# Optimization experiments

Hardware: AMD Instinct MI355X
Metric: run time of the kernel (lower is better)

## Reference

```python
import jax, jax.numpy as jnp
import numpy as np

N = 50000      # nodes
E = 800000     # edges (avg degree 16)
IN, HID, OUT = 128, 256, 64
G = 500        # graphs in the batch (100 nodes each)
NEG_SLOPE = 0.01
EPS = 1e-12


def setup_inputs() -> dict:
    key = jax.random.key(0)
    ks = jax.random.split(key, 9)
    x = jax.random.normal(ks[0], (N, IN), jnp.float32)
    edge_index = jax.random.randint(ks[1], (2, E), 0, N, dtype=jnp.int32)
    # sorted segment ids with every graph present (100 nodes per graph)
    batch = jnp.repeat(jnp.arange(G, dtype=jnp.int32), N // G)
    def lin(k, fan_in, fan_out):
        s = 1.0 / np.sqrt(fan_in)
        kw, kb = jax.random.split(k)
        W = jax.random.uniform(kw, (fan_in, fan_out), jnp.float32, -s, s)
        b = jax.random.uniform(kb, (fan_out,), jnp.float32, -s, s)
        return W, b
    W1, b1 = lin(ks[2], IN, HID)
    W2, b2 = lin(ks[3], HID, HID)
    W3, b3 = lin(ks[4], HID, OUT)
    return {"x": x, "edge_index": edge_index, "batch": batch,
            "W1": W1, "b1": b1, "W2": W2, "b2": b2, "W3": W3, "b3": b3}


def _sage_conv(x, edge_index, W, b):
    # SAGEConv(aggr='add', root_weight=False, normalize=True):
    # gather source features, scatter-add to targets, linear, L2 normalize.
    src, dst = edge_index[0], edge_index[1]
    agg = jax.ops.segment_sum(x[src], dst, num_segments=x.shape[0])  # [N, d_in]
    out = agg @ W + b                                                 # [N, d_out]
    nrm = jnp.linalg.norm(out, axis=-1, keepdims=True)
    return out / jnp.maximum(nrm, EPS)


def reference(x, edge_index, batch, W1, b1, W2, b2, W3, b3):
    h = _sage_conv(x, edge_index, W1, b1)
    h = jax.nn.leaky_relu(h, NEG_SLOPE)          # dropout p=0 -> identity
    h = _sage_conv(h, edge_index, W2, b2)
    h = jax.nn.leaky_relu(h, NEG_SLOPE)
    h = _sage_conv(h, edge_index, W3, b3)
    # get_zero_nodes: first node of each graph (batch sorted, all G present)
    mask = jnp.concatenate([jnp.ones((1,), bool), batch[1:] != batch[:-1]])
    first_idx = jnp.nonzero(mask, size=G)[0]
    return h[first_idx]                          # [G, OUT]
```

## Files before the change

kernel.cpp:

```cpp
#include <hip/hip_runtime.h>

#define N_NODES 50000
#define E_EDGES 800000
#define IN_DIM  128
#define HID_DIM 256
#define OUT_DIM 64
#define G_GRAPHS 500
#define CAP 64
#define NBINS 196
#define BINCAP 5120

typedef __attribute__((ext_vector_type(8))) short short8;
typedef __attribute__((ext_vector_type(4))) float float4v;

__device__ __forceinline__ float bf2f(unsigned short u) {
  union { unsigned int i; float f; } c; c.i = ((unsigned int)u) << 16; return c.f;
}
__device__ __forceinline__ unsigned short f2bf(float f) {
  union { float f; unsigned int i; } c; c.f = f;
  unsigned int x = c.i;
  x += 0x7FFFu + ((x >> 16) & 1u);
  return (unsigned short)(x >> 16);
}
__device__ __forceinline__ unsigned int fbits(float f) {
  union { float f; unsigned int i; } c; c.f = f; return c.i;
}
__device__ __forceinline__ float bits2f(unsigned int u) {
  union { unsigned int i; float f; } c; c.i = u; return c.f;
}


__global__ __launch_bounds__(256) void prep1(
    const int* __restrict__ src, const int* __restrict__ dst,
    const int* __restrict__ batch,
    const float* __restrict__ x,
    const float* __restrict__ W1, const float* __restrict__ W2,
    unsigned int* __restrict__ binbuf, int* __restrict__ bin_next,
    int* __restrict__ first_node,
    unsigned short* __restrict__ xb,
    unsigned short* __restrict__ W1t, unsigned short* __restrict__ W2t) {
  const int b = blockIdx.x, tid = threadIdx.x;
  if (b < 200) {
    __shared__ int cnt[NBINS];
    __shared__ int gbase[NBINS];
    for (int i = tid; i < NBINS; i += 256) cnt[i] = 0;
    __syncthreads();
    const int base = b * 4096;
    unsigned int pk[16]; int bp[16];
#pragma unroll
    for (int u = 0; u < 16; ++u) {
      const int e = base + u * 256 + tid;
      bp[u] = -1;
      if (e < E_EDGES) {
        const int d = dst[e];
        const int s = src[e];
        const int bin = d >> 8;
        const int pos = atomicAdd(&cnt[bin], 1);
        pk[u] = ((unsigned int)(d & 255) << 16) | (unsigned int)s;
        bp[u] = (bin << 16) | pos;
      }
    }
    __syncthreads();
    for (int i = tid; i < NBINS; i += 256)
      gbase[i] = atomicAdd(&bin_next[i], cnt[i]);
    __syncthreads();
#pragma unroll
    for (int u = 0; u < 16; ++u) {
      if (bp[u] >= 0) {
        const int bin = bp[u] >> 16, pos = bp[u] & 0xFFFF;
        const int idx = gbase[bin] + pos;
        if (idx < BINCAP) binbuf[bin * BINCAP + idx] = pk[u];
      }
    }
  } else if (b < 6450) {
    const int t = (b - 200) * 256 + tid;
    const int i = t * 4;
    const float4 v = *(const float4*)(x + i);
    ushort4 u;
    u.x = f2bf(v.x); u.y = f2bf(v.y); u.z = f2bf(v.z); u.w = f2bf(v.w);
    *(ushort4*)(xb + i) = u;
    if (t < N_NODES) {
      if (t == 0 || batch[t] != batch[t - 1]) first_node[batch[t]] = t;
    }
  } else {
    const int t = (b - 6450) * 256 + tid;
    if (t < 8192) {
      const int n = t >> 5, k0 = (t & 31) * 4;
      ushort4 o;
      o.x = f2bf(W1[(k0 + 0) * 256 + n]);
      o.y = f2bf(W1[(k0 + 1) * 256 + n]);
      o.z = f2bf(W1[(k0 + 2) * 256 + n]);
      o.w = f2bf(W1[(k0 + 3) * 256 + n]);
      *(ushort4*)&W1t[n * 128 + k0] = o;
    } else {
      const int v2 = t - 8192;
      const int n = v2 >> 6, k0 = (v2 & 63) * 4;
      ushort4 o;
      o.x = f2bf(W2[(k0 + 0) * 256 + n]);
      o.y = f2bf(W2[(k0 + 1) * 256 + n]);
      o.z = f2bf(W2[(k0 + 2) * 256 + n]);
      o.w = f2bf(W2[(k0 + 3) * 256 + n]);
      *(ushort4*)&W2t[n * 256 + k0] = o;
    }
  }
}


__global__ __launch_bounds__(512) void prep2(
    const unsigned int* __restrict__ binbuf, const int* __restrict__ bin_next,
    int* __restrict__ deg, unsigned short* __restrict__ srcs) {
  __shared__ unsigned short img[256 * CAP];
  __shared__ int cnt[256];
  const int tid = threadIdx.x;
  const int bin = blockIdx.x;
  if (tid < 256) cnt[tid] = 0;
  __syncthreads();
  const int total = min(bin_next[bin], BINCAP);
  const unsigned int* bb = binbuf + bin * BINCAP;
  for (int i = tid; i < total; i += 512) {
    const unsigned int pk = bb[i];
    const int nl = pk >> 16;
    const int pos = atomicAdd(&cnt[nl], 1);
    if (pos < CAP) img[(nl << 6) + pos] = (unsigned short)(pk & 0xFFFFu);
  }
  __syncthreads();
  const int node0 = bin << 8;
  const int nend = min(N_NODES, node0 + 256);
  if (tid < 256 && node0 + tid < nend) deg[node0 + tid] = cnt[tid];
  const int nwords = (nend - node0) * 32;
  unsigned int* dstw = (unsigned int*)(srcs + ((size_t)node0 << 6));
  const unsigned int* srcw = (const unsigned int*)img;
  for (int i = tid; i < nwords; i += 512) dstw[i] = srcw[i];
}


__global__ __launch_bounds__(64) void build_list2(
    const int* __restrict__ deg, const unsigned short* __restrict__ srcs,
    const int* __restrict__ first_node,
    unsigned char* __restrict__ need1, int* __restrict__ list2,
    int* __restrict__ cnt2) {
  const int g = blockIdx.x;
  const int lane = threadIdx.x;
  const int node = first_node[g];
  const int cnt = min(deg[node], CAP);
  int s = 0;
  if (lane < cnt) s = srcs[(node << 6) + lane];
  const unsigned long long m = __ballot(lane < cnt);
  int base = 0;
  if (lane == 0) base = atomicAdd(cnt2, __popcll(m));
  base = __shfl(base, 0);
  if (lane < cnt) {
    list2[base + lane] = s;
    const int c2 = min(deg[s], CAP);
    for (int q = 0; q < c2; ++q) need1[srcs[(s << 6) + q]] = 1;
  }
}

__global__ __launch_bounds__(256) void compact_list1(
    const unsigned char* __restrict__ need1,
    int* __restrict__ list1, int* __restrict__ cnt1) {
  __shared__ int wbase[4];
  const int tid = threadIdx.x;
  const int lane = tid & 63;
  const int wv = tid >> 6;
  const int i = blockIdx.x * 256 + tid;
  const bool f = (i < N_NODES) && need1[i];
  const unsigned long long m = __ballot(f);
  if (lane == 0) wbase[wv] = __popcll(m);
  __syncthreads();
  if (tid == 0) {
    const int t0 = wbase[0], t1 = wbase[1], t2 = wbase[2], t3 = wbase[3];
    const int b = atomicAdd(cnt1, t0 + t1 + t2 + t3);
    wbase[0] = b; wbase[1] = b + t0; wbase[2] = b + t0 + t1; wbase[3] = b + t0 + t1 + t2;
  }
  __syncthreads();
  if (f) list1[wbase[wv] + __popcll(m & ((1ull << lane) - 1ull))] = i;
}


template<int K>
__global__ __launch_bounds__(512, 8) void fused_layer(
    const unsigned short* __restrict__ H,
    const int* __restrict__ deg, const unsigned short* __restrict__ srcs,
    const unsigned short* __restrict__ Wt,
    const float* __restrict__ bias,
    unsigned short* __restrict__ Hout,
    const int* __restrict__ nodelist,
    const int* __restrict__ pcount)
{
  constexpr int M = 256;
  constexpr int TN = 16;
  constexpr int VPT = K / 64;
  constexpr int LDK = K + 8;
  __shared__ unsigned short a_hi[TN][LDK];
  __shared__ unsigned short a_lo[TN][LDK];
  __shared__ float ssq_tot[TN];
  __shared__ int nid_s[TN];
  const int tid = threadIdx.x;
  const int lane = tid & 63;
  const int wv = tid >> 6;

  const int total = __builtin_amdgcn_readfirstlane(*pcount);
  if (blockIdx.x * TN >= total) return;

  if (tid < TN) {
    int gi = blockIdx.x * TN + tid;
    if (gi >= total) gi = total - 1;
    nid_s[tid] = nodelist[gi];
    ssq_tot[tid] = 0.f;
  }
  __syncthreads();

  const unsigned short* hb = H + lane * VPT;
  const int node0 = __builtin_amdgcn_readfirstlane(nid_s[2 * wv]);
  const int node1 = __builtin_amdgcn_readfirstlane(nid_s[2 * wv + 1]);
  const int cnt0 = __builtin_amdgcn_readfirstlane(min(deg[node0], CAP));
  const int cnt1 = __builtin_amdgcn_readfirstlane(min(deg[node1], CAP));
  int idx0 = 0, idx1 = 0;
  if (lane < cnt0) idx0 = srcs[(node0 << 6) + lane];
  if (lane < cnt1) idx1 = srcs[(node1 << 6) + lane];

#pragma unroll
  for (int i = 0; i < 2; ++i) {
    const int nn = 2 * wv + i;
    const int cnt = i ? cnt1 : cnt0;
    const int idx = i ? idx1 : idx0;

    float acc[VPT];
#pragma unroll
    for (int j = 0; j < VPT; ++j) acc[j] = 0.f;

    int j = 0;
    for (; j + 16 <= cnt; j += 16) {
      int s[16];
#pragma unroll
      for (int u = 0; u < 16; ++u) s[u] = __builtin_amdgcn_readlane(idx, j + u);
      if constexpr (VPT == 4) {
        ushort4 r[16];
#pragma unroll
        for (int u = 0; u < 16; ++u) r[u] = *(const ushort4*)(hb + s[u] * K);
#pragma unroll
        for (int u = 0; u < 16; ++u) {
          acc[0] += bf2f(r[u].x); acc[1] += bf2f(r[u].y);
          acc[2] += bf2f(r[u].z); acc[3] += bf2f(r[u].w);
        }
      } else {
        ushort2 r[16];
#pragma unroll
        for (int u = 0; u < 16; ++u) r[u] = *(const ushort2*)(hb + s[u] * K);
#pragma unroll
        for (int u = 0; u < 16; ++u) {
          acc[0] += bf2f(r[u].x); acc[1] += bf2f(r[u].y);
        }
      }
    }
    for (; j < cnt; j += 8) {
      int s[8]; float w[8];
#pragma unroll
      for (int u = 0; u < 8; ++u) {
        const int q = j + u;
        const int qm = (q < cnt) ? q : (cnt - 1);
        s[u] = __builtin_amdgcn_readlane(idx, qm);
        w[u] = (q < cnt) ? 1.f : 0.f;
      }
      if constexpr (VPT == 4) {
        ushort4 r[8];
#pragma unroll
        for (int u = 0; u < 8; ++u) r[u] = *(const ushort4*)(hb + s[u] * K);
#pragma unroll
        for (int u = 0; u < 8; ++u) {
          acc[0] = fmaf(w[u], bf2f(r[u].x), acc[0]);
          acc[1] = fmaf(w[u], bf2f(r[u].y), acc[1]);
          acc[2] = fmaf(w[u], bf2f(r[u].z), acc[2]);
          acc[3] = fmaf(w[u], bf2f(r[u].w), acc[3]);
        }
      } else {
        ushort2 r[8];
#pragma unroll
        for (int u = 0; u < 8; ++u) r[u] = *(const ushort2*)(hb + s[u] * K);
#pragma unroll
        for (int u = 0; u < 8; ++u) {
          acc[0] = fmaf(w[u], bf2f(r[u].x), acc[0]);
          acc[1] = fmaf(w[u], bf2f(r[u].y), acc[1]);
        }
      }
    }

    unsigned short h[VPT], l[VPT];
#pragma unroll
    for (int jj = 0; jj < VPT; ++jj) {
      const unsigned int u = fbits(acc[jj]);
      h[jj] = (unsigned short)(u >> 16);
      const float res = acc[jj] - bits2f(u & 0xFFFF0000u);
      l[jj] = (unsigned short)(fbits(res) >> 16);
    }
    if constexpr (VPT == 4) {
      *(ushort4*)&a_hi[nn][lane * 4] = make_ushort4(h[0], h[1], h[2], h[3]);
      *(ushort4*)&a_lo[nn][lane * 4] = make_ushort4(l[0], l[1], l[2], l[3]);
    } else {
      *(ushort2*)&a_hi[nn][lane * 2] = make_ushort2(h[0], h[1]);
      *(ushort2*)&a_lo[nn][lane * 2] = make_ushort2(l[0], l[1]);
    }
  }
  __syncthreads();

  const int g = lane >> 4;
  const int lc = lane & 15;
  float4v dacc0 = (float4v){0.f, 0.f, 0.f, 0.f};
  float4v dacc1 = (float4v){0.f, 0.f, 0.f, 0.f};
  const unsigned short* W0 = Wt + (size_t)(wv * 16 + lc) * K + g * 8;
  const unsigned short* W1r = Wt + (size_t)((wv + 8) * 16 + lc) * K + g * 8;
#pragma unroll
  for (int ks = 0; ks < K / 32; ++ks) {
    const short8 ah = *(const short8*)&a_hi[lc][ks * 32 + g * 8];
    const short8 al = *(const short8*)&a_lo[lc][ks * 32 + g * 8];
    const short8 b0 = *(const short8*)(W0 + ks * 32);
    const short8 b1 = *(const short8*)(W1r + ks * 32);
    dacc0 = __builtin_amdgcn_mfma_f32_16x16x32_bf16(ah, b0, dacc0, 0, 0, 0);
    dacc0 = __builtin_amdgcn_mfma_f32_16x16x32_bf16(al, b0, dacc0, 0, 0, 0);
    dacc1 = __builtin_amdgcn_mfma_f32_16x16x32_bf16(ah, b1, dacc1, 0, 0, 0);
    dacc1 = __builtin_amdgcn_mfma_f32_16x16x32_bf16(al, b1, dacc1, 0, 0, 0);
  }

  const float bn0 = bias[wv * 16 + lc];
  const float bn1 = bias[(wv + 8) * 16 + lc];
  float4v o0 = dacc0 + bn0;
  float4v o1 = dacc1 + bn1;
  float sq[4];
#pragma unroll
  for (int r = 0; r < 4; ++r) sq[r] = o0[r] * o0[r] + o1[r] * o1[r];
#pragma unroll
  for (int off = 1; off < 16; off <<= 1) {
#pragma unroll
    for (int r = 0; r < 4; ++r) sq[r] += __shfl_xor(sq[r], off);
  }
  if (lc == 0) {
#pragma unroll
    for (int r = 0; r < 4; ++r) atomicAdd(&ssq_tot[g * 4 + r], sq[r]);
  }
  __syncthreads();

#pragma unroll
  for (int r = 0; r < 4; ++r) {
    const float inv = 1.f / fmaxf(sqrtf(ssq_tot[g * 4 + r]), 1e-12f);
    float v0 = o0[r] * inv;
    float v1 = o1[r] * inv;
    v0 = (v0 >= 0.f) ? v0 : 0.01f * v0;
    v1 = (v1 >= 0.f) ? v1 : 0.01f * v1;
    const int nd = nid_s[g * 4 + r];
    Hout[(size_t)nd * M + wv * 16 + lc] = f2bf(v0);
    Hout[(size_t)nd * M + (wv + 8) * 16 + lc] = f2bf(v1);
  }
}


__global__ __launch_bounds__(64) void layer3_kernel(
    const unsigned short* __restrict__ H2,
    const int* __restrict__ deg, const unsigned short* __restrict__ srcs,
    const int* __restrict__ first_node,
    const float* __restrict__ W,
    const float* __restrict__ bias,
    float* __restrict__ out)
{
  __shared__ float a_s[HID_DIM];
  const int g = blockIdx.x;
  const int lane = threadIdx.x;
  const int node = first_node[g];
  const int cnt = min(deg[node], CAP);
  float acc[4] = {0.f, 0.f, 0.f, 0.f};
  for (int p = 0; p < cnt; ++p) {
    const int s = srcs[(node << 6) + p];
    const ushort4 u = *(const ushort4*)(H2 + (size_t)s * HID_DIM + lane * 4);
    acc[0] += bf2f(u.x); acc[1] += bf2f(u.y); acc[2] += bf2f(u.z); acc[3] += bf2f(u.w);
  }
  *(float4*)&a_s[lane * 4] = make_float4(acc[0], acc[1], acc[2], acc[3]);
  __syncthreads();
  float o = bias[lane];
#pragma unroll 8
  for (int k = 0; k < HID_DIM; ++k) o += a_s[k] * W[k * OUT_DIM + lane];
  float ss = o * o;
#pragma unroll
  for (int off = 32; off > 0; off >>= 1) ss += __shfl_xor(ss, off);
  const float inv = 1.f / fmaxf(sqrtf(ss), 1e-12f);
  out[(size_t)g * OUT_DIM + lane] = o * inv;
}


extern "C" void kernel_launch(void* const* d_in, const int* in_sizes, int n_in,
                              void* d_out, int out_size, void* d_ws, size_t ws_size,
                              hipStream_t stream) {
  (void)in_sizes; (void)n_in; (void)out_size; (void)ws_size;
  const float* x   = (const float*)d_in[0];
  const int* ei    = (const int*)d_in[1];
  const int* batch = (const int*)d_in[2];
  const float* W1  = (const float*)d_in[3];
  const float* b1  = (const float*)d_in[4];
  const float* W2  = (const float*)d_in[5];
  const float* b2  = (const float*)d_in[6];
  const float* W3  = (const float*)d_in[7];
  const float* b3  = (const float*)d_in[8];
  const int* src = ei;
  const int* dst = ei + E_EDGES;

  char* ws = (char*)d_ws;
  size_t off = 0;
  auto alloc = [&](size_t bytes) {
    void* p = ws + off;
    off = (off + bytes + 255) & ~(size_t)255;
    return p;
  };
  unsigned char* need1 = (unsigned char*)alloc((size_t)N_NODES);
  int* cnts    = (int*)alloc(256);
  int* bin_next= (int*)alloc((size_t)NBINS * 4);
  const size_t zero_len = off;
  int* cnt1 = cnts;
  int* cnt2 = cnts + 1;

  int* deg    = (int*)alloc((size_t)N_NODES * 4);
  unsigned short* srcs = (unsigned short*)alloc((size_t)N_NODES * CAP * 2);
  int* first  = (int*)alloc((size_t)G_GRAPHS * 4);
  int* list1  = (int*)alloc((size_t)N_NODES * 4);
  int* list2  = (int*)alloc((size_t)G_GRAPHS * CAP * 4);
  unsigned int* binbuf = (unsigned int*)alloc((size_t)NBINS * BINCAP * 4);
  unsigned short* W1t = (unsigned short*)alloc((size_t)256 * 128 * 2);
  unsigned short* W2t = (unsigned short*)alloc((size_t)256 * 256 * 2);
  unsigned short* h2 = (unsigned short*)alloc((size_t)N_NODES * HID_DIM * 2);
  unsigned short* xb = h2;
  unsigned short* h1 = (unsigned short*)alloc((size_t)N_NODES * HID_DIM * 2);

  hipMemsetAsync(need1, 0, zero_len, stream);

  prep1<<<6546, 256, 0, stream>>>(src, dst, batch, x, W1, W2,
                                  binbuf, bin_next, first, xb, W1t, W2t);
  prep2<<<NBINS, 512, 0, stream>>>(binbuf, bin_next, deg, srcs);

  build_list2<<<G_GRAPHS, 64, 0, stream>>>(deg, srcs, first, need1, list2, cnt2);
  compact_list1<<<(N_NODES + 255) / 256, 256, 0, stream>>>(need1, list1, cnt1);

  fused_layer<IN_DIM><<<N_NODES / 16, 512, 0, stream>>>(xb, deg, srcs, W1t, b1, h1,
                                                        list1, cnt1);
  fused_layer<HID_DIM><<<(G_GRAPHS * CAP) / 16, 512, 0, stream>>>(h1, deg, srcs, W2t, b2, h2,
                                                                  list2, cnt2);
  layer3_kernel<<<G_GRAPHS, 64, 0, stream>>>(h2, deg, srcs, first, W3, b3, (float*)d_out);
}
```

Measured before the change: 202.5 us.

## Drop layer-1 node pruning, fold list2 build into prep2, interleave neighbor gathers

Removes the build_list2 and compact_list1 kernels. Layer 1 now runs densely over all nodes rather than only the 2-hop-needed subset, and the list of neighbors of each graph's first node is built inside prep2 from its shared-memory adjacency image. The layer-1 gather loop also processes both of a wave's nodes together in 16-edge chunks so more loads are in flight. This trades two small serial kernel launches and their dependency chain for possibly more layer-1 work, depending on how many nodes the 2-hop set covered.

```diff
diff --git a/kernel.cpp b/kernel.cpp
--- a/kernel.cpp
+++ b/kernel.cpp
@@ -36,7 +36,7 @@
     const float* __restrict__ x,
     const float* __restrict__ W1, const float* __restrict__ W2,
     unsigned int* __restrict__ binbuf, int* __restrict__ bin_next,
-    int* __restrict__ first_node,
+    int* __restrict__ first_node, unsigned char* __restrict__ is_first,
     unsigned short* __restrict__ xb,
     unsigned short* __restrict__ W1t, unsigned short* __restrict__ W2t) {
   const int b = blockIdx.x, tid = threadIdx.x;
@@ -80,7 +80,9 @@
     u.x = f2bf(v.x); u.y = f2bf(v.y); u.z = f2bf(v.z); u.w = f2bf(v.w);
     *(ushort4*)(xb + i) = u;
     if (t < N_NODES) {
-      if (t == 0 || batch[t] != batch[t - 1]) first_node[batch[t]] = t;
+      const int fl = (t == 0 || batch[t] != batch[t - 1]) ? 1 : 0;
+      is_first[t] = (unsigned char)fl;
+      if (fl) first_node[batch[t]] = t;
     }
   } else {
     const int t = (b - 6450) * 256 + tid;
@@ -108,7 +110,9 @@
 
 __global__ __launch_bounds__(512) void prep2(
     const unsigned int* __restrict__ binbuf, const int* __restrict__ bin_next,
-    int* __restrict__ deg, unsigned short* __restrict__ srcs) {
+    const unsigned char* __restrict__ is_first,
+    int* __restrict__ deg, unsigned short* __restrict__ srcs,
+    int* __restrict__ list2, int* __restrict__ cnt2) {
   __shared__ unsigned short img[256 * CAP];
   __shared__ int cnt[256];
   const int tid = threadIdx.x;
@@ -126,7 +130,14 @@
   __syncthreads();
   const int node0 = bin << 8;
   const int nend = min(N_NODES, node0 + 256);
-  if (tid < 256 && node0 + tid < nend) deg[node0 + tid] = cnt[tid];
+  if (tid < 256 && node0 + tid < nend) {
+    const int c = min(cnt[tid], CAP);
+    deg[node0 + tid] = cnt[tid];
+    if (is_first[node0 + tid]) {
+      const int base = atomicAdd(cnt2, c);
+      for (int q = 0; q < c; ++q) list2[base + q] = (int)img[(tid << 6) + q];
+    }
+  }
   const int nwords = (nend - node0) * 32;
   unsigned int* dstw = (unsigned int*)(srcs + ((size_t)node0 << 6));
   const unsigned int* srcw = (const unsigned int*)img;
@@ -134,51 +145,7 @@
 }
 
 
-__global__ __launch_bounds__(64) void build_list2(
-    const int* __restrict__ deg, const unsigned short* __restrict__ srcs,
-    const int* __restrict__ first_node,
-    unsigned char* __restrict__ need1, int* __restrict__ list2,
-    int* __restrict__ cnt2) {
-  const int g = blockIdx.x;
-  const int lane = threadIdx.x;
-  const int node = first_node[g];
-  const int cnt = min(deg[node], CAP);
-  int s = 0;
-  if (lane < cnt) s = srcs[(node << 6) + lane];
-  const unsigned long long m = __ballot(lane < cnt);
-  int base = 0;
-  if (lane == 0) base = atomicAdd(cnt2, __popcll(m));
-  base = __shfl(base, 0);
-  if (lane < cnt) {
-    list2[base + lane] = s;
-    const int c2 = min(deg[s], CAP);
-    for (int q = 0; q < c2; ++q) need1[srcs[(s << 6) + q]] = 1;
-  }
-}
-
-__global__ __launch_bounds__(256) void compact_list1(
-    const unsigned char* __restrict__ need1,
-    int* __restrict__ list1, int* __restrict__ cnt1) {
-  __shared__ int wbase[4];
-  const int tid = threadIdx.x;
-  const int lane = tid & 63;
-  const int wv = tid >> 6;
-  const int i = blockIdx.x * 256 + tid;
-  const bool f = (i < N_NODES) && need1[i];
-  const unsigned long long m = __ballot(f);
-  if (lane == 0) wbase[wv] = __popcll(m);
-  __syncthreads();
-  if (tid == 0) {
-    const int t0 = wbase[0], t1 = wbase[1], t2 = wbase[2], t3 = wbase[3];
-    const int b = atomicAdd(cnt1, t0 + t1 + t2 + t3);
-    wbase[0] = b; wbase[1] = b + t0; wbase[2] = b + t0 + t1; wbase[3] = b + t0 + t1 + t2;
-  }
-  __syncthreads();
-  if (f) list1[wbase[wv] + __popcll(m & ((1ull << lane) - 1ull))] = i;
-}
-
-
-template<int K>
+template<int K, bool LIST>
 __global__ __launch_bounds__(512, 8) void fused_layer(
     const unsigned short* __restrict__ H,
     const int* __restrict__ deg, const unsigned short* __restrict__ srcs,
@@ -200,13 +167,20 @@
   const int lane = tid & 63;
   const int wv = tid >> 6;
 
-  const int total = __builtin_amdgcn_readfirstlane(*pcount);
-  if (blockIdx.x * TN >= total) return;
+  int total = N_NODES;
+  if constexpr (LIST) {
+    total = __builtin_amdgcn_readfirstlane(*pcount);
+    if (blockIdx.x * TN >= total) return;
+  }
 
   if (tid < TN) {
     int gi = blockIdx.x * TN + tid;
-    if (gi >= total) gi = total - 1;
-    nid_s[tid] = nodelist[gi];
+    if constexpr (LIST) {
+      if (gi >= total) gi = total - 1;
+      nid_s[tid] = nodelist[gi];
+    } else {
+      nid_s[tid] = gi;
+    }
     ssq_tot[tid] = 0.f;
   }
   __syncthreads();
@@ -220,17 +194,41 @@
   if (lane < cnt0) idx0 = srcs[(node0 << 6) + lane];
   if (lane < cnt1) idx1 = srcs[(node1 << 6) + lane];
 
+  float acc0[VPT], acc1[VPT];
+#pragma unroll
+  for (int q = 0; q < VPT; ++q) { acc0[q] = 0.f; acc1[q] = 0.f; }
+  int j0 = 0, j1 = 0;
+
+  if constexpr (VPT == 2) {
+    while (j0 + 16 <= cnt0 && j1 + 16 <= cnt1) {
+      int s0[16], s1[16];
+#pragma unroll
+      for (int u = 0; u < 16; ++u) {
+        s0[u] = __builtin_amdgcn_readlane(idx0, j0 + u);
+        s1[u] = __builtin_amdgcn_readlane(idx1, j1 + u);
+      }
+      ushort2 r0[16], r1[16];
+#pragma unroll
+      for (int u = 0; u < 16; ++u) r0[u] = *(const ushort2*)(hb + s0[u] * K);
+#pragma unroll
+      for (int u = 0; u < 16; ++u) r1[u] = *(const ushort2*)(hb + s1[u] * K);
+#pragma unroll
+      for (int u = 0; u < 16; ++u) {
+        acc0[0] += bf2f(r0[u].x); acc0[1] += bf2f(r0[u].y);
+        acc1[0] += bf2f(r1[u].x); acc1[1] += bf2f(r1[u].y);
+      }
+      j0 += 16; j1 += 16;
+    }
+  }
+
 #pragma unroll
   for (int i = 0; i < 2; ++i) {
     const int nn = 2 * wv + i;
     const int cnt = i ? cnt1 : cnt0;
     const int idx = i ? idx1 : idx0;
-
-    float acc[VPT];
-#pragma unroll
-    for (int j = 0; j < VPT; ++j) acc[j] = 0.f;
-
-    int j = 0;
+    float (&acc)[VPT] = i ? acc1 : acc0;
+    int j = i ? j1 : j0;
+
     for (; j + 16 <= cnt; j += 16) {
       int s[16];
 #pragma unroll
@@ -409,17 +407,15 @@
     off = (off + bytes + 255) & ~(size_t)255;
     return p;
   };
-  unsigned char* need1 = (unsigned char*)alloc((size_t)N_NODES);
   int* cnts    = (int*)alloc(256);
   int* bin_next= (int*)alloc((size_t)NBINS * 4);
   const size_t zero_len = off;
-  int* cnt1 = cnts;
-  int* cnt2 = cnts + 1;
+  int* cnt2 = cnts;
 
   int* deg    = (int*)alloc((size_t)N_NODES * 4);
   unsigned short* srcs = (unsigned short*)alloc((size_t)N_NODES * CAP * 2);
   int* first  = (int*)alloc((size_t)G_GRAPHS * 4);
-  int* list1  = (int*)alloc((size_t)N_NODES * 4);
+  unsigned char* is_first = (unsigned char*)alloc((size_t)N_NODES);
   int* list2  = (int*)alloc((size_t)G_GRAPHS * CAP * 4);
   unsigned int* binbuf = (unsigned int*)alloc((size_t)NBINS * BINCAP * 4);
   unsigned short* W1t = (unsigned short*)alloc((size_t)256 * 128 * 2);
@@ -428,18 +424,15 @@
   unsigned short* xb = h2;
   unsigned short* h1 = (unsigned short*)alloc((size_t)N_NODES * HID_DIM * 2);
 
-  hipMemsetAsync(need1, 0, zero_len, stream);
+  hipMemsetAsync(cnts, 0, zero_len, stream);
 
   prep1<<<6546, 256, 0, stream>>>(src, dst, batch, x, W1, W2,
-                                  binbuf, bin_next, first, xb, W1t, W2t);
-  prep2<<<NBINS, 512, 0, stream>>>(binbuf, bin_next, deg, srcs);
-
-  build_list2<<<G_GRAPHS, 64, 0, stream>>>(deg, srcs, first, need1, list2, cnt2);
-  compact_list1<<<(N_NODES + 255) / 256, 256, 0, stream>>>(need1, list1, cnt1);
-
-  fused_layer<IN_DIM><<<N_NODES / 16, 512, 0, stream>>>(xb, deg, srcs, W1t, b1, h1,
-                                                        list1, cnt1);
-  fused_layer<HID_DIM><<<(G_GRAPHS * CAP) / 16, 512, 0, stream>>>(h1, deg, srcs, W2t, b2, h2,
-                                                                  list2, cnt2);
+                                  binbuf, bin_next, first, is_first, xb, W1t, W2t);
+  prep2<<<NBINS, 512, 0, stream>>>(binbuf, bin_next, is_first, deg, srcs, list2, cnt2);
+
+  fused_layer<IN_DIM, false><<<N_NODES / 16, 512, 0, stream>>>(
+      xb, deg, srcs, W1t, b1, h1, nullptr, nullptr);
+  fused_layer<HID_DIM, true><<<(G_GRAPHS * CAP) / 16, 512, 0, stream>>>(
+      h1, deg, srcs, W2t, b2, h2, list2, cnt2);
   layer3_kernel<<<G_GRAPHS, 64, 0, stream>>>(h2, deg, srcs, first, W3, b3, (float*)d_out);
 }
```

After: 197.1 us. -2.7%, faster.
